# Performance work log

Measured on AMD Instinct MI355X. Metric: run time of the kernel, lower is better.

Reference implementation:

```python
import jax, jax.numpy as jnp
import numpy as np
from jax import lax

_OFFS = [(dx, dy, dz) for dx in (-1, 0, 1) for dy in (-1, 0, 1) for dz in (-1, 0, 1)]


def _cell(coords, S):
    # padded linear cell index: spatial dims get +1 shift into an (S+2)^3 grid so
    # +/-1 neighbor offsets never leave the slab
    P = S + 2
    return ((coords[:, 0] * P + coords[:, 1] + 1) * P + coords[:, 2] + 1) * P + coords[:, 3] + 1


def _build_grid(coords, S, n_slabs):
    g = jnp.full((n_slabs * (S + 2) ** 3,), -1, jnp.int32)
    return g.at[_cell(coords, S)].set(jnp.arange(coords.shape[0], dtype=jnp.int32))


def _forward(voxel_coords, voxel_feats, centroid_scores, offsets, bg_desc, W_desc, mixer_W, mixer_b, S, B):
    N, C = voxel_feats.shape
    TAU, PEAK_THRESH, K = 0.1, 0.2, 128
    # ---------- _revoxelize (torch: @no_grad) ----------
    off4 = jnp.concatenate([jnp.zeros((N, 1), jnp.int32), offsets.astype(jnp.int32)], 1)
    new_coords = voxel_coords + off4
    key = _cell(new_coords, S)                       # sphash equivalent (coords are unique per cell)
    order = jnp.argsort(key)
    ks = key[order]
    newflag = jnp.concatenate([jnp.ones((1,), bool), ks[1:] != ks[:-1]])
    sid = jnp.cumsum(newflag.astype(jnp.int32)) - 1
    seg = jnp.zeros((N,), jnp.int32).at[order].set(sid)      # idx_query (unique -> fixed N segments)
    counts = jax.ops.segment_sum(jnp.ones((N,), jnp.float32), seg, num_segments=N)
    mean_coords = jax.ops.segment_sum(new_coords.astype(jnp.float32), seg, num_segments=N) / jnp.maximum(counts, 1.0)[:, None]
    clus_coords = mean_coords.astype(jnp.int32)              # spvoxelize(...).int()
    valid_clus = counts > 0
    clus_coords = clus_coords.at[:, 0].set(jnp.where(valid_clus, clus_coords[:, 0], B))  # park empty segs in spare slab
    cpv = counts[seg][:, None]                                # counts gathered per voxel
    clus_sum = jax.ops.segment_sum(voxel_feats / cpv, seg, num_segments=N)  # scatter_sum(F/counts)
    # submanifold 3x3x3 avg pool over cluster sites
    cgrid = _build_grid(clus_coords, S, B + 1)
    acc = jnp.zeros_like(clus_sum)
    cnt = jnp.zeros((N, 1), jnp.float32)
    for off in _OFFS:
        nc = clus_coords + jnp.array([0, *off], jnp.int32)
        j = cgrid[_cell(nc, S)]
        v = (j >= 0)[:, None]
        acc = acc + jnp.where(v, clus_sum[jnp.maximum(j, 0)], 0.0)
        cnt = cnt + v.astype(jnp.float32)
    pooled = acc / jnp.maximum(cnt, 1.0)
    cluster_feats = lax.stop_gradient(pooled[seg])            # [N, C], gathered back per voxel
    cluster_scores = lax.stop_gradient(cpv)                   # [N, 1]
    # ---------- union + mixer 3x3x3 subm conv ----------
    vgrid = _build_grid(voxel_coords, S, B)
    featsAB = jnp.concatenate([centroid_scores, cluster_scores], 1)  # same coords -> hash union is identity match
    mix = jnp.broadcast_to(mixer_b, (N, 1)).astype(jnp.float32)
    for kth, off in enumerate(_OFFS):
        nc = voxel_coords + jnp.array([0, *off], jnp.int32)
        j = vgrid[_cell(nc, S)]
        v = (j >= 0)[:, None]
        mix = mix + jnp.where(v, featsAB[jnp.maximum(j, 0)] @ mixer_W[kth], 0.0)
    refined = jax.nn.sigmoid(mix)                             # [N, 1]
    # ---------- _find_centroid_peaks (torch: @no_grad), NMS via subm max-pool ----------
    score = lax.stop_gradient(refined[:, 0])
    m = score > TAU
    val = jnp.where(m, score, -jnp.inf)                       # submanifold active set = masked voxels
    hmax = jnp.full((N,), -jnp.inf, jnp.float32)
    for off in _OFFS:
        nc = voxel_coords + jnp.array([0, *off], jnp.int32)
        j = vgrid[_cell(nc, S)]
        nv = jnp.where(j >= 0, val[jnp.maximum(j, 0)], -jnp.inf)
        hmax = jnp.maximum(hmax, nv)
    peak = m & (hmax == score) & (score > PEAK_THRESH)
    top_vals, top_idx = lax.top_k(jnp.where(peak, score, -1.0), K)
    valid_peak = top_vals > 0.0
    conf = jnp.where(valid_peak, top_vals, 0.0)[:, None]      # [K, 1]
    peak_feats = jnp.where(valid_peak[:, None], cluster_feats[top_idx], 0.0)
    # ---------- descriptors + instance logits ----------
    voxel_desc = jax.nn.relu(cluster_feats @ W_desc)          # 1x1x1 sparse conv + ReLU == pointwise linear
    peak_desc = conf * jax.nn.relu(peak_feats @ W_desc)       # [K, D]
    descriptors = jnp.concatenate([bg_desc, peak_desc], 0)    # [K+1, D]
    instance = (voxel_desc @ descriptors.T)[seg]              # gather-matmul then index_select(inv_map)
    return refined, conf, instance


def setup_inputs() -> dict:
    rng = np.random.default_rng(0)
    S, B, N = 96, 2, 200000
    LATENT, DESC = 64, 32
    C = LATENT + 3
    inner = S - 8  # keep coords in [4, S-5] so coords + offsets in [-4,4] stay in-bounds
    per = N // B
    coords = []
    for b in range(B):
        lin = rng.choice(inner ** 3, size=per, replace=False)  # unique voxel coords per batch
        x = lin // (inner * inner)
        y = (lin // inner) % inner
        z = lin % inner
        coords.append(np.stack([np.full(per, b), x + 4, y + 4, z + 4], 1))
    coords = jnp.asarray(np.concatenate(coords, 0).astype(np.int32))
    ks = jax.random.split(jax.random.key(0), 8)
    return dict(
        voxel_coords=coords,
        voxel_feats=jax.random.normal(ks[0], (N, C), jnp.float32),
        centroid_scores=jax.random.uniform(ks[1], (N, 1), dtype=jnp.float32),
        offsets=jax.random.randint(ks[2], (N, 3), -4, 5).astype(jnp.float32),
        bg_desc=jax.random.normal(ks[3], (1, DESC), jnp.float32) * 0.02,
        W_desc=jax.random.normal(ks[4], (C, DESC), jnp.float32) * 0.05,
        mixer_W=jax.random.normal(ks[5], (27, 2, 1), jnp.float32) * 0.5,
        mixer_b=jnp.zeros((1,), jnp.float32),
        spatial_size=S,
        batch_size=B,
    )


def reference(voxel_coords, voxel_feats, centroid_scores, offsets, bg_desc, W_desc, mixer_W, mixer_b, spatial_size, batch_size):
    return _forward(voxel_coords, voxel_feats, centroid_scores, offsets, bg_desc, W_desc, mixer_W, mixer_b, int(spatial_size), int(batch_size))
```

## Files before the change

kernel.cpp:

```cpp
#include <hip/hip_runtime.h>
#include <stdint.h>

#define S_   96
#define P_   98
#define NB_  2
#define GSZ  (NB_*P_*P_*P_)
#define C_   67
#define CP_  68
#define D_   32
#define KTOP 128
#define SELCAP 1024

typedef unsigned int u32;
typedef unsigned long long u64;

struct Ctrl {
  u64 prefix;
  int n_peaks;
  int kk;
  int selctr;
  int nseg;
};

__device__ __forceinline__ int cell4(int b, int x, int y, int z) {
  return ((b*P_ + x + 1)*P_ + y + 1)*P_ + z + 1;
}

__global__ __launch_bounds__(256) void k_clear(int4* __restrict__ rank, int4* __restrict__ cgrid,
                                               int4* __restrict__ vgrid, int4* __restrict__ cnts, int N) {
  const int R4 = GSZ/4;
  const int N4 = N/4;
  int idx = blockIdx.x*256 + threadIdx.x;
  int stride = gridDim.x*256;
  const int4 z = make_int4(0,0,0,0), m1 = make_int4(-1,-1,-1,-1);
  for (int i = idx; i < R4; i += stride) { rank[i] = z; cgrid[i] = m1; vgrid[i] = m1; }
  for (int i = idx; i < N4; i += stride) cnts[i] = z;
}

__global__ __launch_bounds__(1024) void k_init(Ctrl* c, int* __restrict__ hist) {
  int t = threadIdx.x;
  for (int i = t; i < 65536; i += 1024) hist[i] = 0;
  if (t == 0) { c->prefix = 0ull; c->n_peaks = 0; c->kk = KTOP; c->selctr = 0; }
}

__global__ __launch_bounds__(256) void k_key(const int* __restrict__ vc, const float* __restrict__ offs,
                                             int* __restrict__ keyA, int* __restrict__ rank,
                                             int* __restrict__ vgrid, int N) {
  int i = blockIdx.x*256 + threadIdx.x;
  if (i >= N) return;
  const int4 q = ((const int4*)vc)[i];
  int ox = (int)offs[3*i], oy = (int)offs[3*i+1], oz = (int)offs[3*i+2];
  int k = cell4(q.x, q.y+ox, q.z+oy, q.w+oz);
  keyA[i] = k;
  rank[k] = 1;
  vgrid[cell4(q.x, q.y, q.z, q.w)] = i;
}

#define SC_TPB 256
#define SC_EPT 8
#define SC_EPB (SC_TPB*SC_EPT)

__global__ __launch_bounds__(SC_TPB) void k_scan1(int* __restrict__ a, int* __restrict__ bsum, int n) {
  __shared__ int sd[SC_TPB];
  int t = threadIdx.x;
  int base = blockIdx.x*SC_EPB + t*SC_EPT;
  int x[SC_EPT]; int s = 0;
  #pragma unroll
  for (int e = 0; e < SC_EPT; ++e) { int idx = base+e; x[e] = (idx < n) ? a[idx] : 0; s += x[e]; }
  sd[t] = s; __syncthreads();
  for (int off = 1; off < SC_TPB; off <<= 1) {
    int v = (t >= off) ? sd[t-off] : 0; __syncthreads(); sd[t] += v; __syncthreads();
  }
  int run = sd[t] - s;
  #pragma unroll
  for (int e = 0; e < SC_EPT; ++e) { int idx = base+e; if (idx < n) a[idx] = run; run += x[e]; }
  if (t == SC_TPB-1) bsum[blockIdx.x] = sd[t];
}

__global__ __launch_bounds__(SC_TPB) void k_scan2(int* __restrict__ bsum, int nb, Ctrl* ctrl) {
  __shared__ int sd[SC_TPB];
  int t = threadIdx.x;
  int x[4]; int s = 0;
  #pragma unroll
  for (int e = 0; e < 4; ++e) { int idx = t*4+e; x[e] = (idx < nb) ? bsum[idx] : 0; s += x[e]; }
  sd[t] = s; __syncthreads();
  for (int off = 1; off < SC_TPB; off <<= 1) {
    int v = (t >= off) ? sd[t-off] : 0; __syncthreads(); sd[t] += v; __syncthreads();
  }
  int run = sd[t] - s;
  #pragma unroll
  for (int e = 0; e < 4; ++e) { int idx = t*4+e; if (idx < nb) bsum[idx] = run; run += x[e]; }
  if (t == SC_TPB-1) ctrl->nseg = sd[t];
}

__global__ __launch_bounds__(SC_TPB) void k_scan3(int* __restrict__ a, const int* __restrict__ bsum, int n) {
  int add = bsum[blockIdx.x];
  int base = blockIdx.x*SC_EPB + threadIdx.x*SC_EPT;
  #pragma unroll
  for (int e = 0; e < SC_EPT; ++e) { int idx = base+e; if (idx < n) a[idx] += add; }
}

__global__ __launch_bounds__(256) void k_seg(const int* __restrict__ keyA, const int* __restrict__ rank,
                                             int* __restrict__ seg, int* __restrict__ cnts,
                                             int* __restrict__ cgrid, int* __restrict__ ckey, int N) {
  int i = blockIdx.x*256 + threadIdx.x;
  if (i >= N) return;
  int k = keyA[i];
  int s = rank[k];
  seg[i] = s;
  atomicAdd(&cnts[s], 1);
  cgrid[k] = s;
  ckey[s] = k;
}

__global__ __launch_bounds__(256) void k_fabzero(const int* __restrict__ seg, const int* __restrict__ cnts,
                                                 const float* __restrict__ cent, float2* __restrict__ fab,
                                                 int* __restrict__ g2, float* __restrict__ clussum, int N) {
  int i = blockIdx.x*256 + threadIdx.x;
  if (i >= N) return;
  int s = seg[i];
  int c = cnts[s];
  fab[i] = make_float2(cent[i], (float)c);
  g2[i] = seg[s];
  if (c > 1) {
    float4* row = (float4*)(clussum + (size_t)s*CP_);
    const float4 fz = make_float4(0.f,0.f,0.f,0.f);
    #pragma unroll
    for (int k = 0; k < CP_/4; ++k) row[k] = fz;
  }
}

__global__ __launch_bounds__(256) void k_accum(const int* __restrict__ seg, const int* __restrict__ cnts,
                                               const float* __restrict__ feats,
                                               float* __restrict__ clussum, int N) {
  int t = threadIdx.x;
  int i = blockIdx.x*4 + (t >> 6);
  if (i >= N) return;
  int lane = t & 63;
  int s = seg[i];
  int cnt = cnts[s];
  float inv = 1.0f/(float)cnt;
  const float* fr = feats + (size_t)i*C_;
  float* dst = clussum + (size_t)s*CP_;
  float v0 = fr[lane]*inv;
  float v1 = (lane < C_-64) ? fr[64+lane]*inv : 0.f;
  if (cnt == 1) {
    dst[lane] = v0;
    if (lane < C_-64) dst[64+lane] = v1;
  } else {
    atomicAdd(&dst[lane], v0);
    if (lane < C_-64) atomicAdd(&dst[64+lane], v1);
  }
}

__global__ __launch_bounds__(64) void k_pool(const Ctrl* __restrict__ ctrl,
                                             const int* __restrict__ ckey, const int* __restrict__ cgrid,
                                             const float* __restrict__ clussum, const float* __restrict__ Wd,
                                             float* __restrict__ V) {
  int nseg = ctrl->nseg;
  int s0 = blockIdx.x*2;
  if (s0 >= nseg) return;
  int t = threadIdx.x;
  int half = t >> 5, l = t & 31;
  int s = s0 + half;
  bool segok = (s < nseg);
  int j = -1;
  if (segok && l < 27) {
    int dx = l/9 - 1, dy = (l/3)%3 - 1, dz = l%3 - 1;
    j = cgrid[ckey[s] + (dx*P_ + dy)*P_ + dz];
  }
  float a0 = 0.f, a1 = 0.f, b0 = 0.f, b1 = 0.f;
  int nva = 0, nvb = 0;
  #pragma unroll
  for (int k = 0; k < 27; ++k) {
    int ja = __shfl(j, k);
    int jb = __shfl(j, 32 + k);
    if (ja >= 0) {
      const float* r = clussum + (size_t)ja*CP_;
      a0 += r[t];
      if (t < 3) a1 += r[64 + t];
      ++nva;
    }
    if (jb >= 0) {
      const float* r = clussum + (size_t)jb*CP_;
      b0 += r[t];
      if (t < 3) b1 += r[64 + t];
      ++nvb;
    }
  }
  __shared__ float pL[2][CP_];
  float inva = 1.f/(float)(nva > 0 ? nva : 1);
  pL[0][t] = a0*inva;
  if (t < 3) pL[0][64 + t] = a1*inva;
  if (s0 + 1 < nseg) {
    float invb = 1.f/(float)(nvb > 0 ? nvb : 1);
    pL[1][t] = b0*invb;
    if (t < 3) pL[1][64 + t] = b1*invb;
  }
  __syncthreads();
  if (segok) {
    const float* p = pL[half];
    float acc = 0.f;
    #pragma unroll
    for (int c = 0; c < C_; ++c) acc += p[c] * Wd[c*D_ + l];
    V[(size_t)s*D_ + l] = fmaxf(acc, 0.f);
  }
}

__global__ __launch_bounds__(256) void k_mixer(const int* __restrict__ vc, const int* __restrict__ vgrid,
                                               const float2* __restrict__ fab, const float* __restrict__ mW,
                                               const float* __restrict__ mB, float* __restrict__ out, int N) {
  int i = blockIdx.x*256 + threadIdx.x;
  if (i >= N) return;
  const int4 q = ((const int4*)vc)[i];
  int bc = cell4(q.x, q.y, q.z, q.w);
  float mix = mB[0];
  #pragma unroll
  for (int k = 0; k < 27; ++k) {
    int dx = k/9 - 1, dy = (k/3)%3 - 1, dz = k%3 - 1;
    int j = vgrid[bc + (dx*P_ + dy)*P_ + dz];
    int jc = (j >= 0) ? j : 0;
    float2 f = fab[jc];
    float msk = (j >= 0) ? 1.f : 0.f;
    mix += msk * (f.x*mW[2*k] + f.y*mW[2*k+1]);
  }
  out[i] = 1.f/(1.f + expf(-mix));
}

__global__ __launch_bounds__(256) void k_peak(const int* __restrict__ vc, const int* __restrict__ vgrid,
                                              const float* __restrict__ out, Ctrl* __restrict__ ctrl,
                                              u64* __restrict__ cand, int N) {
  int i = blockIdx.x*256 + threadIdx.x;
  if (i >= N) return;
  const float NINF = __int_as_float(0xff800000);
  float sc = out[i];
  const int4 q = ((const int4*)vc)[i];
  int bc = cell4(q.x, q.y, q.z, q.w);
  float hmax = NINF;
  #pragma unroll
  for (int k = 0; k < 27; ++k) {
    int dx = k/9 - 1, dy = (k/3)%3 - 1, dz = k%3 - 1;
    int j = vgrid[bc + (dx*P_ + dy)*P_ + dz];
    int jc = (j >= 0) ? j : 0;
    float sj = out[jc];
    float vj = (j >= 0 && sj > 0.1f) ? sj : NINF;
    hmax = fmaxf(hmax, vj);
  }
  if (sc > 0.2f && hmax == sc) {
    int pos = atomicAdd(&ctrl->n_peaks, 1);
    cand[pos] = ((u64)__float_as_uint(sc) << 32) | (u32)(~(u32)i);
  }
}

__global__ __launch_bounds__(256) void k_hist(const u64* __restrict__ cand, const Ctrl* __restrict__ ctrl,
                                              int* __restrict__ hist, int shift) {
  int idx = blockIdx.x*256 + threadIdx.x;
  if (idx >= ctrl->n_peaks) return;
  u64 key = cand[idx];
  if (shift != 48 && (((key ^ ctrl->prefix) >> (shift + 16)) != 0)) return;
  atomicAdd(&hist[(int)((key >> shift) & 0xFFFF)], 1);
}

__global__ __launch_bounds__(1024) void k_scansel(int* __restrict__ hist, Ctrl* __restrict__ ctrl, int shift) {
  __shared__ int sd[1024];
  int t = threadIdx.x;
  int kk = ctrl->kk;
  int lo = 65536 - (t+1)*64;
  int s = 0;
  for (int b = lo; b < lo+64; ++b) s += hist[b];
  sd[t] = s; __syncthreads();
  for (int off = 1; off < 1024; off <<= 1) {
    int v = (t >= off) ? sd[t-off] : 0; __syncthreads(); sd[t] += v; __syncthreads();
  }
  int before = sd[t] - s;
  if (before < kk && before + s >= kk) {
    int cum = before;
    for (int b = lo+63; b >= lo; --b) {
      int h = hist[b];
      if (cum + h >= kk) { ctrl->prefix |= ((u64)(u32)b) << shift; ctrl->kk = kk - cum; break; }
      cum += h;
    }
  }
  __syncthreads();
  for (int b = lo; b < lo+64; ++b) hist[b] = 0;
}

__global__ __launch_bounds__(256) void k_collect(const u64* __restrict__ cand, Ctrl* __restrict__ ctrl,
                                                 u64* __restrict__ sel) {
  int idx = blockIdx.x*256 + threadIdx.x;
  int np = ctrl->n_peaks;
  if (idx >= np) return;
  u64 key = cand[idx];
  bool take = (np <= KTOP) ? true : ((u32)(key >> 32) >= (u32)(ctrl->prefix >> 32));
  if (take) { int pos = atomicAdd(&ctrl->selctr, 1); if (pos < SELCAP) sel[pos] = key; }
}

__global__ __launch_bounds__(SELCAP) void k_rank(const u64* __restrict__ sel, const Ctrl* __restrict__ ctrl,
                                                 float* __restrict__ out, int* __restrict__ topidx, int N) {
  __shared__ u64 sk[SELCAP];
  int t = threadIdx.x;
  int ns = ctrl->selctr; if (ns > SELCAP) ns = SELCAP;
  if (t < KTOP) { out[N + t] = 0.f; topidx[t] = -1; }
  sk[t] = (t < ns) ? sel[t] : 0ull;
  __syncthreads();
  if (t < ns) {
    u64 my = sk[t];
    int r = 0;
    for (int m = 0; m < ns; ++m) r += (sk[m] > my) ? 1 : 0;
    if (r < KTOP) {
      out[N + r] = __uint_as_float((u32)(my >> 32));
      topidx[r]  = (int)~(u32)(my & 0xFFFFFFFFull);
    }
  }
}

__global__ void k_desc(const int* __restrict__ topidx, const int* __restrict__ seg,
                       const float* __restrict__ V, const float* __restrict__ bg,
                       const float* __restrict__ outc, float* __restrict__ descg, int N) {
  int b = blockIdx.x; int d = threadIdx.x;
  if (b == 0) { descg[d] = bg[d]; return; }
  int r = b - 1;
  int ti = topidx[r];
  float v = 0.f;
  if (ti >= 0) v = outc[N + r] * V[(size_t)seg[ti]*D_ + d];
  descg[b*D_ + d] = v;
}

#define VPB 32
__global__ __launch_bounds__(256) void k_inst(const int* __restrict__ g2, const float* __restrict__ V,
                                              const float* __restrict__ descg, float* __restrict__ out, int N) {
  __shared__ __align__(16) float ds[129*36];
  __shared__ __align__(16) float us[VPB*36];
  __shared__ int gs[VPB];
  int tid = threadIdx.x;
  for (int idx = tid; idx < 129*D_; idx += 256) { int j = idx >> 5, d = idx & 31; ds[j*36 + d] = descg[idx]; }
  int v0 = blockIdx.x*VPB;
  if (tid < VPB) { int v = v0 + tid; gs[tid] = (v < N) ? g2[v] : -1; }
  __syncthreads();
  for (int idx = tid; idx < VPB*D_; idx += 256) {
    int v = idx >> 5, d = idx & 31; int g = gs[v];
    us[v*36 + d] = (g >= 0) ? V[(size_t)g*D_ + d] : 0.f;
  }
  __syncthreads();
  int tx = tid & 31, ty = tid >> 5;
  const float* usb = us + ty*4*36;
  float acc[4][4];
  #pragma unroll
  for (int a = 0; a < 4; ++a)
    #pragma unroll
    for (int b = 0; b < 4; ++b) acc[a][b] = 0.f;
  float a128[4] = {0.f, 0.f, 0.f, 0.f};
  #pragma unroll
  for (int d4 = 0; d4 < 8; ++d4) {
    float4 uv[4];
    #pragma unroll
    for (int k = 0; k < 4; ++k) uv[k] = *(const float4*)(usb + k*36 + d4*4);
    #pragma unroll
    for (int r = 0; r < 4; ++r) {
      float4 dv = *(const float4*)(ds + (tx + 32*r)*36 + d4*4);
      #pragma unroll
      for (int k = 0; k < 4; ++k)
        acc[k][r] += uv[k].x*dv.x + uv[k].y*dv.y + uv[k].z*dv.z + uv[k].w*dv.w;
    }
    if (tx == 0) {
      float4 dv = *(const float4*)(ds + 128*36 + d4*4);
      #pragma unroll
      for (int k = 0; k < 4; ++k)
        a128[k] += uv[k].x*dv.x + uv[k].y*dv.y + uv[k].z*dv.z + uv[k].w*dv.w;
    }
  }
  #pragma unroll
  for (int k = 0; k < 4; ++k) {
    int v = v0 + ty*4 + k;
    if (v < N) {
      float* o = out + (size_t)v*129;
      #pragma unroll
      for (int r = 0; r < 4; ++r) o[tx + 32*r] = acc[k][r];
      if (tx == 0) o[128] = a128[k];
    }
  }
}

extern "C" void kernel_launch(void* const* d_in, const int* in_sizes, int n_in,
                              void* d_out, int out_size, void* d_ws, size_t ws_size,
                              hipStream_t stream) {
  const int*   vc    = (const int*)d_in[0];
  const float* feats = (const float*)d_in[1];
  const float* cent  = (const float*)d_in[2];
  const float* offs  = (const float*)d_in[3];
  const float* bg    = (const float*)d_in[4];
  const float* Wd    = (const float*)d_in[5];
  const float* mW    = (const float*)d_in[6];
  const float* mB    = (const float*)d_in[7];
  int N = in_sizes[2];

  float* out = (float*)d_out;

  uint8_t* base = (uint8_t*)d_ws;
  size_t off = 0;
  auto carve = [&](size_t bytes) -> void* {
    off = (off + 255) & ~(size_t)255;
    void* r = base + off; off += bytes; return r;
  };
  Ctrl*   ctrl    = (Ctrl*)  carve(sizeof(Ctrl));
  int*    keyA    = (int*)   carve((size_t)N*4);
  int*    seg     = (int*)   carve((size_t)N*4);
  int*    cnts    = (int*)   carve((size_t)N*4);
  int*    ckey    = (int*)   carve((size_t)N*4);
  int*    g2      = (int*)   carve((size_t)N*4);
  float2* fab     = (float2*)carve((size_t)N*8);
  int*    rank    = (int*)   carve((size_t)GSZ*4);
  int*    bsum    = (int*)   carve(1024*4);
  int*    cgrid   = (int*)   carve((size_t)GSZ*4);
  int*    vgrid   = (int*)   carve((size_t)GSZ*4);
  float*  clussum = (float*) carve((size_t)N*CP_*4);
  float*  V       = (float*) carve((size_t)N*D_*4);
  u64*    cand    = (u64*)   carve((size_t)N*8);
  int*    hist    = (int*)   carve(65536*4);
  u64*    sel     = (u64*)   carve(SELCAP*8);
  int*    topidx  = (int*)   carve(KTOP*4);
  float*  descg   = (float*) carve(129*D_*4);

  int nb256 = (N + 255)/256;
  int nscan = (GSZ + SC_EPB - 1)/SC_EPB;
  int nclr  = (GSZ/4 + 255)/256;

  k_clear<<<nclr, 256, 0, stream>>>((int4*)rank, (int4*)cgrid, (int4*)vgrid, (int4*)cnts, N);
  k_init<<<1, 1024, 0, stream>>>(ctrl, hist);

  k_key<<<nb256, 256, 0, stream>>>(vc, offs, keyA, rank, vgrid, N);
  k_scan1<<<nscan, SC_TPB, 0, stream>>>(rank, bsum, GSZ);
  k_scan2<<<1, SC_TPB, 0, stream>>>(bsum, nscan, ctrl);
  k_scan3<<<nscan, SC_TPB, 0, stream>>>(rank, bsum, GSZ);
  k_seg<<<nb256, 256, 0, stream>>>(keyA, rank, seg, cnts, cgrid, ckey, N);

  k_fabzero<<<nb256, 256, 0, stream>>>(seg, cnts, cent, fab, g2, clussum, N);
  k_accum<<<(N + 3)/4, 256, 0, stream>>>(seg, cnts, feats, clussum, N);
  k_pool<<<(N + 1)/2, 64, 0, stream>>>(ctrl, ckey, cgrid, clussum, Wd, V);

  k_mixer<<<nb256, 256, 0, stream>>>(vc, vgrid, fab, mW, mB, out, N);
  k_peak<<<nb256, 256, 0, stream>>>(vc, vgrid, out, ctrl, cand, N);

  for (int shift = 48; shift >= 32; shift -= 16) {
    k_hist<<<nb256, 256, 0, stream>>>(cand, ctrl, hist, shift);
    k_scansel<<<1, 1024, 0, stream>>>(hist, ctrl, shift);
  }
  k_collect<<<nb256, 256, 0, stream>>>(cand, ctrl, sel);
  k_rank<<<1, SELCAP, 0, stream>>>(sel, ctrl, out, topidx, N);

  k_desc<<<KTOP + 1, D_, 0, stream>>>(topidx, seg, V, bg, out, descg, N);
  k_inst<<<(N + VPB - 1)/VPB, 256, 0, stream>>>(g2, V, descg, out + N + KTOP, N);
}
```

Measured before the change: 708.4 us.

## Restructure instance-descriptor kernel with transposed descriptors and vectorized output stores

k_inst now stores the descriptor table transposed in shared memory, so each lane reads float4 descriptor columns and accumulates four outputs per voxel as float4. Output rows are written with 16-byte vector stores. Each block now handles 128 voxels with 512 threads instead of 32 voxels with 256 threads, which spreads the one-time descriptor load per block over more voxels. The float4 stores land on addresses that are not 16-byte aligned because rows are 129 floats long, and k_scan2's loop bound is hardcoded to 1024, which may add barrier iterations.

```diff
diff --git a/kernel.cpp b/kernel.cpp
--- a/kernel.cpp
+++ b/kernel.cpp
@@ -84,7 +84,7 @@
   #pragma unroll
   for (int e = 0; e < 4; ++e) { int idx = t*4+e; x[e] = (idx < nb) ? bsum[idx] : 0; s += x[e]; }
   sd[t] = s; __syncthreads();
-  for (int off = 1; off < SC_TPB; off <<= 1) {
+  for (int off = 1; off < 1024; off <<= 1) {
     int v = (t >= off) ? sd[t-off] : 0; __syncthreads(); sd[t] += v; __syncthreads();
   }
   int run = sd[t] - s;
@@ -326,57 +326,66 @@
   descg[b*D_ + d] = v;
 }
 
-#define VPB 32
-__global__ __launch_bounds__(256) void k_inst(const int* __restrict__ g2, const float* __restrict__ V,
+#define VPB 128
+__global__ __launch_bounds__(512) void k_inst(const int* __restrict__ g2, const float* __restrict__ V,
                                               const float* __restrict__ descg, float* __restrict__ out, int N) {
-  __shared__ __align__(16) float ds[129*36];
-  __shared__ __align__(16) float us[VPB*36];
+  __shared__ __align__(16) float dsT[32*136];
+  __shared__ __align__(16) float ds128[32];
+  __shared__ __align__(16) float us[VPB*D_];
   __shared__ int gs[VPB];
   int tid = threadIdx.x;
-  for (int idx = tid; idx < 129*D_; idx += 256) { int j = idx >> 5, d = idx & 31; ds[j*36 + d] = descg[idx]; }
+  for (int idx = tid; idx < 129*D_; idx += 512) {
+    int c = idx >> 5, d = idx & 31;
+    float val = descg[idx];
+    if (c == 128) ds128[d] = val;
+    else dsT[d*136 + c] = val;
+  }
   int v0 = blockIdx.x*VPB;
   if (tid < VPB) { int v = v0 + tid; gs[tid] = (v < N) ? g2[v] : -1; }
   __syncthreads();
-  for (int idx = tid; idx < VPB*D_; idx += 256) {
+  for (int idx = tid; idx < VPB*D_; idx += 512) {
     int v = idx >> 5, d = idx & 31; int g = gs[v];
-    us[v*36 + d] = (g >= 0) ? V[(size_t)g*D_ + d] : 0.f;
+    us[idx] = (g >= 0) ? V[(size_t)g*D_ + d] : 0.f;
   }
   __syncthreads();
-  int tx = tid & 31, ty = tid >> 5;
-  const float* usb = us + ty*4*36;
-  float acc[4][4];
-  #pragma unroll
-  for (int a = 0; a < 4; ++a)
+  int w = tid >> 6, lane = tid & 63;
+  int h = lane >> 5, tx = lane & 31;
+  #pragma unroll
+  for (int s = 0; s < 2; ++s) {
+    int vb = w*16 + s*8 + h*4;
+    float4 acc[4];
     #pragma unroll
-    for (int b = 0; b < 4; ++b) acc[a][b] = 0.f;
-  float a128[4] = {0.f, 0.f, 0.f, 0.f};
-  #pragma unroll
-  for (int d4 = 0; d4 < 8; ++d4) {
-    float4 uv[4];
+    for (int k = 0; k < 4; ++k) acc[k] = make_float4(0.f,0.f,0.f,0.f);
+    float a128[4] = {0.f, 0.f, 0.f, 0.f};
     #pragma unroll
-    for (int k = 0; k < 4; ++k) uv[k] = *(const float4*)(usb + k*36 + d4*4);
+    for (int d4 = 0; d4 < 8; ++d4) {
+      float4 uv[4];
+      #pragma unroll
+      for (int k = 0; k < 4; ++k) uv[k] = *(const float4*)(us + (vb+k)*D_ + d4*4);
+      #pragma unroll
+      for (int dd = 0; dd < 4; ++dd) {
+        float4 dv = *(const float4*)(dsT + (size_t)(d4*4+dd)*136 + tx*4);
+        #pragma unroll
+        for (int k = 0; k < 4; ++k) {
+          float u = (dd==0) ? uv[k].x : (dd==1) ? uv[k].y : (dd==2) ? uv[k].z : uv[k].w;
+          acc[k].x += u*dv.x; acc[k].y += u*dv.y; acc[k].z += u*dv.z; acc[k].w += u*dv.w;
+        }
+      }
+      if (tx == 0) {
+        float4 e = *(const float4*)(ds128 + d4*4);
+        #pragma unroll
+        for (int k = 0; k < 4; ++k)
+          a128[k] += uv[k].x*e.x + uv[k].y*e.y + uv[k].z*e.z + uv[k].w*e.w;
+      }
+    }
     #pragma unroll
-    for (int r = 0; r < 4; ++r) {
-      float4 dv = *(const float4*)(ds + (tx + 32*r)*36 + d4*4);
-      #pragma unroll
-      for (int k = 0; k < 4; ++k)
-        acc[k][r] += uv[k].x*dv.x + uv[k].y*dv.y + uv[k].z*dv.z + uv[k].w*dv.w;
-    }
-    if (tx == 0) {
-      float4 dv = *(const float4*)(ds + 128*36 + d4*4);
-      #pragma unroll
-      for (int k = 0; k < 4; ++k)
-        a128[k] += uv[k].x*dv.x + uv[k].y*dv.y + uv[k].z*dv.z + uv[k].w*dv.w;
-    }
-  }
-  #pragma unroll
-  for (int k = 0; k < 4; ++k) {
-    int v = v0 + ty*4 + k;
-    if (v < N) {
-      float* o = out + (size_t)v*129;
-      #pragma unroll
-      for (int r = 0; r < 4; ++r) o[tx + 32*r] = acc[k][r];
-      if (tx == 0) o[128] = a128[k];
+    for (int k = 0; k < 4; ++k) {
+      int gv = v0 + vb + k;
+      if (gv < N) {
+        float* o = out + (size_t)gv*129;
+        *(float4*)(o + tx*4) = acc[k];
+        if (tx == 0) o[128] = a128[k];
+      }
     }
   }
 }
@@ -449,5 +458,5 @@
   k_rank<<<1, SELCAP, 0, stream>>>(sel, ctrl, out, topidx, N);
 
   k_desc<<<KTOP + 1, D_, 0, stream>>>(topidx, seg, V, bg, out, descg, N);
-  k_inst<<<(N + VPB - 1)/VPB, 256, 0, stream>>>(g2, V, descg, out + N + KTOP, N);
-}
+  k_inst<<<(N + VPB - 1)/VPB, 512, 0, stream>>>(g2, V, descg, out + N + KTOP, N);
+}
```

Result: no change. 696.6 us (-1.7%).
